# Kernel tuning notes

Hardware: AMD Instinct MI355X
Metric: run time of the kernel (lower is better)

The kernel has to match this reference:

```python
import jax, jax.numpy as jnp
import numpy as np

N_NODES = 100000
IN_CH = 128
OUT_CH = 128
N_EDGES = 1700000


def setup_inputs() -> dict:
    key = jax.random.key(0)
    k_x, k_e, k_w = jax.random.split(key, 3)
    x = jax.random.normal(k_x, (N_NODES, IN_CH), dtype=jnp.float32)
    # edges: one self-loop per node (guarantees deg>=1 for every node),
    # remainder random
    loops = jnp.stack([jnp.arange(N_NODES, dtype=jnp.int64)] * 2)  # [2, N]
    rand = jax.random.randint(k_e, (2, N_EDGES - N_NODES), 0, N_NODES, dtype=jnp.int64)
    edge_index = jnp.concatenate([loops, rand], axis=1)  # [2, E]
    # glorot-uniform weight, zero bias (reset_parameters)
    limit = float(np.sqrt(6.0 / (IN_CH + OUT_CH)))
    weight = jax.random.uniform(k_w, (IN_CH, OUT_CH), dtype=jnp.float32,
                                minval=-limit, maxval=limit)
    bias = jnp.zeros((OUT_CH,), dtype=jnp.float32)
    return {"x": x, "edge_index": edge_index, "weight": weight, "bias": bias}


def reference(x, edge_index, weight, bias):
    row, col = edge_index[0], edge_index[1]
    # deg = bincount(row) over all N nodes
    deg = jax.ops.segment_sum(jnp.ones_like(row, dtype=jnp.float32), row,
                              num_segments=x.shape[0])
    deg_inv_sqrt = deg ** -0.5  # symmetric normalization
    norm = deg_inv_sqrt[row] * deg_inv_sqrt[col]  # [E]
    support = x @ weight  # [N, out]
    msgs = norm[:, None] * support[col]  # [E, out] gather + scale
    out = jax.ops.segment_sum(msgs, row, num_segments=x.shape[0])  # scatter-add
    return out + bias
```

## Files before the change

### kernel.cpp

```cpp
#include <hip/hip_runtime.h>
#include <hip/hip_bf16.h>


#define SCAN_B 256
#define NBLK_P 256
#define BSHIFT 9
#define NPB    512

typedef __attribute__((ext_vector_type(8))) short bf16x8;
typedef __attribute__((ext_vector_type(4))) float f32x4;

__device__ __forceinline__ uint32_t f2bf_rne(float f) {
    uint32_t u = __float_as_uint(f);
    return (u + 0x7fffu + ((u >> 16) & 1u)) >> 16;
}
__device__ __forceinline__ float bf_lo(uint32_t u) { return __uint_as_float(u << 16); }
__device__ __forceinline__ float bf_hi(uint32_t u) { return __uint_as_float(u & 0xffff0000u); }

__device__ __forceinline__ bf16x8 pack8(float4 lo, float4 hi) {
    union { bf16x8 v; ushort u[8]; } r;
    r.u[0] = (ushort)f2bf_rne(lo.x);
    r.u[1] = (ushort)f2bf_rne(lo.y);
    r.u[2] = (ushort)f2bf_rne(lo.z);
    r.u[3] = (ushort)f2bf_rne(lo.w);
    r.u[4] = (ushort)f2bf_rne(hi.x);
    r.u[5] = (ushort)f2bf_rne(hi.y);
    r.u[6] = (ushort)f2bf_rne(hi.z);
    r.u[7] = (ushort)f2bf_rne(hi.w);
    return r.v;
}

__global__ void wconv_kernel(const float* __restrict__ W, ushort* __restrict__ Wt) {
    int t = blockIdx.x * blockDim.x + threadIdx.x;
    int n = t >> 7, k = t & 127;
    Wt[n * 128 + k] = (ushort)f2bf_rne(W[k * 128 + n]);
}

__global__ __launch_bounds__(256) void mfma_gemm(const float* __restrict__ X,
                                                 const ushort* __restrict__ Wt,
                                                 uint32_t* __restrict__ S, int N) {
    const int wave = threadIdx.x >> 6;
    const int lane = threadIdx.x & 63;
    const int c16  = lane & 15;
    const int kg   = lane >> 4;
    const int row0 = blockIdx.x * 128 + wave * 32;

    int rA0 = row0 + c16;
    int rA1 = row0 + 16 + c16;
    if (rA0 >= N) rA0 = N - 1;
    if (rA1 >= N) rA1 = N - 1;

    f32x4 acc[2][8];
#pragma unroll
    for (int m = 0; m < 2; ++m)
#pragma unroll
        for (int cb = 0; cb < 8; ++cb) acc[m][cb] = (f32x4){0.f, 0.f, 0.f, 0.f};

    const float*  xa0 = X + (size_t)rA0 * 128 + kg * 8;
    const float*  xa1 = X + (size_t)rA1 * 128 + kg * 8;
    const ushort* wb  = Wt + kg * 8 + c16 * 128;

#pragma unroll
    for (int kk = 0; kk < 4; ++kk) {
        float4 a0lo = *(const float4*)(xa0 + kk * 32);
        float4 a0hi = *(const float4*)(xa0 + kk * 32 + 4);
        float4 a1lo = *(const float4*)(xa1 + kk * 32);
        float4 a1hi = *(const float4*)(xa1 + kk * 32 + 4);
        bf16x8 A0 = pack8(a0lo, a0hi);
        bf16x8 A1 = pack8(a1lo, a1hi);
#pragma unroll
        for (int cb = 0; cb < 8; ++cb) {
            bf16x8 B = *(const bf16x8*)(wb + (size_t)cb * 16 * 128 + kk * 32);
            acc[0][cb] = __builtin_amdgcn_mfma_f32_16x16x32_bf16(A0, B, acc[0][cb], 0, 0, 0);
            acc[1][cb] = __builtin_amdgcn_mfma_f32_16x16x32_bf16(A1, B, acc[1][cb], 0, 0, 0);
        }
    }
#pragma unroll
    for (int m = 0; m < 2; ++m) {
#pragma unroll
        for (int i = 0; i < 4; ++i) {
            int gr = row0 + m * 16 + kg * 4 + i;
            if (gr < N) {
#pragma unroll
                for (int cb = 0; cb < 4; ++cb) {
                    uint32_t p = f2bf_rne(acc[m][cb][i]) |
                                 (f2bf_rne(acc[m][cb + 4][i]) << 16);
                    S[(size_t)gr * 64 + cb * 16 + c16] = p;
                }
            }
        }
    }
}

__global__ __launch_bounds__(256) void p1_count(const int* __restrict__ row,
                                                int* __restrict__ cnt,
                                                int E, int chunk, int nbuck) {
    __shared__ int h[256];
    const int blk = blockIdx.x, t = threadIdx.x;
    for (int i = t; i < nbuck; i += 256) h[i] = 0;
    __syncthreads();
    int lo = blk * chunk, hi = min(E, lo + chunk);
    for (int e = lo + t; e < hi; e += 256) atomicAdd(&h[row[e] >> BSHIFT], 1);
    __syncthreads();
    for (int b = t; b < nbuck; b += 256) cnt[b * NBLK_P + blk] = h[b];
}

__global__ void scan_block_kernel(const int* __restrict__ in, int* __restrict__ outp,
                                  int* __restrict__ bsum, int M) {
    __shared__ int s[SCAN_B];
    int t = threadIdx.x;
    int g = blockIdx.x * SCAN_B + t;
    int v = (g < M) ? in[g] : 0;
    s[t] = v;
    __syncthreads();
#pragma unroll
    for (int off = 1; off < SCAN_B; off <<= 1) {
        int u = (t >= off) ? s[t - off] : 0;
        __syncthreads();
        s[t] += u;
        __syncthreads();
    }
    if (g < M) outp[g] = s[t] - v;
    if (t == SCAN_B - 1) bsum[blockIdx.x] = s[t];
}

__global__ void scan_bsum_kernel(int* __restrict__ bsum, int NB) {
    __shared__ int s[1024];
    int t = threadIdx.x;
    int v = (t < NB) ? bsum[t] : 0;
    s[t] = v;
    __syncthreads();
#pragma unroll
    for (int off = 1; off < 1024; off <<= 1) {
        int u = (t >= off) ? s[t - off] : 0;
        __syncthreads();
        s[t] += u;
        __syncthreads();
    }
    if (t < NB) bsum[t] = s[t] - v;
}

__global__ void scan_add_kernel(int* __restrict__ outp, const int* __restrict__ bsum, int M) {
    int g = blockIdx.x * blockDim.x + threadIdx.x;
    if (g < M) outp[g] += bsum[g >> 8];
}

__global__ __launch_bounds__(256) void p2_scatter(const int* __restrict__ row,
                                                  const int* __restrict__ col,
                                                  const int* __restrict__ off,
                                                  uint32_t* __restrict__ part,
                                                  int E, int chunk, int nbuck) {
    __shared__ int cur[256];
    const int blk = blockIdx.x, t = threadIdx.x;
    for (int b = t; b < nbuck; b += 256) cur[b] = off[b * NBLK_P + blk];
    __syncthreads();
    int lo = blk * chunk, hi = min(E, lo + chunk);
    for (int e = lo + t; e < hi; e += 256) {
        int r = row[e], c = col[e];
        int pos = atomicAdd(&cur[r >> BSHIFT], 1);
        part[pos] = ((uint32_t)(r & (NPB - 1)) << 17) | (uint32_t)c;
    }
}

__global__ __launch_bounds__(256) void p3_build(const uint32_t* __restrict__ part,
                                                const int* __restrict__ off,
                                                int* __restrict__ rowptr,
                                                float* __restrict__ dis,
                                                int* __restrict__ csr,
                                                int N, int E, int nbuck) {
    __shared__ int hist[NPB];
    __shared__ int lstart[NPB];
    __shared__ int s[256];
    const int b = blockIdx.x, t = threadIdx.x;
    const int base_node = b << BSHIFT;
    const int csr_base  = off[b * NBLK_P];
    const int end_b     = (b == nbuck - 1) ? E : off[(b + 1) * NBLK_P];

    for (int i = t; i < NPB; i += 256) hist[i] = 0;
    __syncthreads();
    for (int e = csr_base + t; e < end_b; e += 256)
        atomicAdd(&hist[part[e] >> 17], 1);
    __syncthreads();

    int a0 = hist[2 * t], a1 = hist[2 * t + 1];
    s[t] = a0 + a1;
    __syncthreads();
    int v = s[t];
#pragma unroll
    for (int o = 1; o < 256; o <<= 1) {
        int u = (t >= o) ? s[t - o] : 0;
        __syncthreads();
        s[t] += u;
        __syncthreads();
    }
    int ex = s[t] - v;
    lstart[2 * t]     = ex;
    lstart[2 * t + 1] = ex + a0;
    __syncthreads();

    for (int i = t; i < NPB; i += 256) {
        int node = base_node + i;
        if (node < N) {
            rowptr[node] = csr_base + lstart[i];
            dis[node]    = rsqrtf((float)hist[i]);
        }
    }
    __syncthreads();
    for (int i = t; i < NPB; i += 256) hist[i] = lstart[i];
    __syncthreads();
    for (int e = csr_base + t; e < end_b; e += 256) {
        uint32_t p = part[e];
        int pos = csr_base + atomicAdd(&hist[p >> 17], 1);
        csr[pos] = (int)(p & 0x1FFFFu);
    }
    if (b == 0 && t == 0) rowptr[N] = E;
}

__global__ __launch_bounds__(256) void gather_kernel(const int* __restrict__ csr,
                                                     const int* __restrict__ rowptr,
                                                     const float* __restrict__ dis,
                                                     const uint32_t* __restrict__ sup,
                                                     const float* __restrict__ bias,
                                                     float* __restrict__ out, int N) {
    int wid  = (blockIdx.x * blockDim.x + threadIdx.x) >> 6;
    int lane = threadIdx.x & 63;
    if (wid >= N) return;
    int begin = rowptr[wid];
    int end   = rowptr[wid + 1];
    float dr  = dis[wid];
    float2 acc;
    acc.x = bias[lane];
    acc.y = bias[64 + lane];

    int j = begin;
    for (; j + 3 < end; j += 4) {
        int c0 = csr[j], c1 = csr[j + 1], c2 = csr[j + 2], c3 = csr[j + 3];
        float n0 = dr * dis[c0], n1 = dr * dis[c1], n2 = dr * dis[c2], n3 = dr * dis[c3];
        uint32_t u0 = sup[(size_t)c0 * 64 + lane];
        uint32_t u1 = sup[(size_t)c1 * 64 + lane];
        uint32_t u2 = sup[(size_t)c2 * 64 + lane];
        uint32_t u3 = sup[(size_t)c3 * 64 + lane];
        acc.x += n0 * bf_lo(u0) + n1 * bf_lo(u1) + n2 * bf_lo(u2) + n3 * bf_lo(u3);
        acc.y += n0 * bf_hi(u0) + n1 * bf_hi(u1) + n2 * bf_hi(u2) + n3 * bf_hi(u3);
    }
    for (; j < end; ++j) {
        int c = csr[j];
        float nrm = dr * dis[c];
        uint32_t u = sup[(size_t)c * 64 + lane];
        acc.x += nrm * bf_lo(u);
        acc.y += nrm * bf_hi(u);
    }
    out[(size_t)wid * 128 + lane]      = acc.x;
    out[(size_t)wid * 128 + 64 + lane] = acc.y;
}

#define GB_M 64
#define GB_KC 32
__global__ __launch_bounds__(256) void gemm_kernel(const float* __restrict__ X,
                                                   const float* __restrict__ W,
                                                   uint32_t* __restrict__ S, int N) {
    __shared__ float sXT[GB_KC][72];
    __shared__ float sW[GB_KC][128];
    const int t  = threadIdx.x;
    const int tx = t & 15;
    const int ty = t >> 4;
    const int bm = blockIdx.x * GB_M;

    float acc[4][8];
#pragma unroll
    for (int i = 0; i < 4; ++i)
#pragma unroll
        for (int j = 0; j < 8; ++j) acc[i][j] = 0.f;

    const int sr = t >> 2;
    const int sc = (t & 3) << 2;

    for (int k0 = 0; k0 < 128; k0 += GB_KC) {
#pragma unroll
        for (int h = 0; h < 2; ++h) {
            int kk = sc + h * 16;
            int gr = bm + sr;
            float4 v = make_float4(0.f, 0.f, 0.f, 0.f);
            if (gr < N) v = *(const float4*)(X + (size_t)gr * 128 + k0 + kk);
            sXT[kk + 0][sr] = v.x;
            sXT[kk + 1][sr] = v.y;
            sXT[kk + 2][sr] = v.z;
            sXT[kk + 3][sr] = v.w;
        }
#pragma unroll
        for (int h = 0; h < 4; ++h) {
            int idx = t + h * 256;
            int wk  = idx >> 5;
            int wo  = (idx & 31) << 2;
            *(float4*)&sW[wk][wo] = *(const float4*)(W + (size_t)(k0 + wk) * 128 + wo);
        }
        __syncthreads();
#pragma unroll
        for (int k = 0; k < GB_KC; ++k) {
            float4 a  = *(const float4*)&sXT[k][ty * 4];
            float4 b0 = *(const float4*)&sW[k][tx * 4];
            float4 b1 = *(const float4*)&sW[k][64 + tx * 4];
            float av[4] = {a.x, a.y, a.z, a.w};
            float bv[8] = {b0.x, b0.y, b0.z, b0.w, b1.x, b1.y, b1.z, b1.w};
#pragma unroll
            for (int i = 0; i < 4; ++i)
#pragma unroll
                for (int j = 0; j < 8; ++j) acc[i][j] += av[i] * bv[j];
        }
        __syncthreads();
    }
#pragma unroll
    for (int i = 0; i < 4; ++i) {
        int gr = bm + ty * 4 + i;
        if (gr < N) {
            uint4 q;
            q.x = f2bf_rne(acc[i][0]) | (f2bf_rne(acc[i][4]) << 16);
            q.y = f2bf_rne(acc[i][1]) | (f2bf_rne(acc[i][5]) << 16);
            q.z = f2bf_rne(acc[i][2]) | (f2bf_rne(acc[i][6]) << 16);
            q.w = f2bf_rne(acc[i][3]) | (f2bf_rne(acc[i][7]) << 16);
            *(uint4*)(S + (size_t)gr * 64 + tx * 4) = q;
        }
    }
}

__global__ void deg_i_kernel(const int* __restrict__ row, int* __restrict__ degi, int E) {
    int g = blockIdx.x * blockDim.x + threadIdx.x;
    if (g < E) atomicAdd(&degi[row[g]], 1);
}
__global__ void rsqrt_i_kernel(const int* __restrict__ degi, float* __restrict__ dis, int N) {
    int g = blockIdx.x * blockDim.x + threadIdx.x;
    if (g < N) dis[g] = rsqrtf((float)degi[g]);
}
__global__ void fill_kernel(const int* __restrict__ row, const int* __restrict__ col,
                            int* __restrict__ start, int* __restrict__ csr, int E) {
    int e = blockIdx.x * blockDim.x + threadIdx.x;
    if (e < E) {
        int pos = atomicAdd(&start[row[e]], 1);
        csr[pos] = col[e];
    }
}
__global__ void rowptr_from_start_kernel(const int* __restrict__ startv,
                                         int* __restrict__ rowptr, int N, int E) {
    int g = blockIdx.x * blockDim.x + threadIdx.x;
    if (g < N) rowptr[g] = startv[g];
    if (g == 0) rowptr[N] = E;
}

extern "C" void kernel_launch(void* const* d_in, const int* in_sizes, int n_in,
                              void* d_out, int out_size, void* d_ws, size_t ws_size,
                              hipStream_t stream) {
    const float* x    = (const float*)d_in[0];
    const int*   ei   = (const int*)d_in[1];
    const float* W    = (const float*)d_in[2];
    const float* bias = (const float*)d_in[3];
    float*       out  = (float*)d_out;

    const int N = in_sizes[0] / 128;
    const int E = in_sizes[1] / 2;
    const int* row = ei;
    const int* col = ei + E;

    const int nbuck = (N + NPB - 1) >> BSHIFT;
    const int M     = nbuck * NBLK_P;
    const int chunk = (E + NBLK_P - 1) / NBLK_P;
    const int NBm   = (M + SCAN_B - 1) / SCAN_B;

    auto al = [](size_t v) { return (v + 511) & ~(size_t)511; };
    size_t o_cnt    = 0;
    size_t o_off    = al(o_cnt + (size_t)M * 4);
    size_t o_bsum   = al(o_off + (size_t)M * 4);
    size_t o_rowptr = al(o_bsum + 4096 * 4);
    size_t o_dis    = al(o_rowptr + ((size_t)N + 1) * 4);
    size_t o_csr    = al(o_dis + (size_t)N * 4);
    size_t o_part   = al(o_csr + (size_t)E * 4);
    size_t o_wt     = al(o_part + (size_t)E * 4);
    size_t o_sup    = al(o_wt + 128 * 128 * 2);
    size_t need     = o_sup + (size_t)N * 256;

    char* ws = (char*)d_ws;

    if (ws_size >= need && nbuck <= 256 && NBm <= 1024 && N <= (1 << 17)) {
        int*      cnt    = (int*)(ws + o_cnt);
        int*      off    = (int*)(ws + o_off);
        int*      bsum   = (int*)(ws + o_bsum);
        int*      rowptr = (int*)(ws + o_rowptr);
        float*    dis    = (float*)(ws + o_dis);
        int*      csr    = (int*)(ws + o_csr);
        uint32_t* part   = (uint32_t*)(ws + o_part);
        ushort*   wt     = (ushort*)(ws + o_wt);
        uint32_t* sup    = (uint32_t*)(ws + o_sup);

        wconv_kernel<<<64, 256, 0, stream>>>(W, wt);
        mfma_gemm<<<(N + 127) / 128, 256, 0, stream>>>(x, wt, sup, N);

        p1_count<<<NBLK_P, 256, 0, stream>>>(row, cnt, E, chunk, nbuck);
        scan_block_kernel<<<NBm, SCAN_B, 0, stream>>>(cnt, off, bsum, M);
        scan_bsum_kernel<<<1, 1024, 0, stream>>>(bsum, NBm);
        scan_add_kernel<<<NBm, SCAN_B, 0, stream>>>(off, bsum, M);
        p2_scatter<<<NBLK_P, 256, 0, stream>>>(row, col, off, part, E, chunk, nbuck);
        p3_build<<<nbuck, 256, 0, stream>>>(part, off, rowptr, dis, csr, N, E, nbuck);

        long long gthreads = (long long)N * 64;
        gather_kernel<<<(int)((gthreads + 255) / 256), 256, 0, stream>>>(
            csr, rowptr, dis, sup, bias, out, N);
    } else {
        size_t f_degi   = 0;
        size_t f_dis    = al(f_degi + (size_t)N * 4);
        size_t f_start  = al(f_dis + (size_t)N * 4);
        size_t f_rowptr = al(f_start + (size_t)N * 4);
        size_t f_bsum   = al(f_rowptr + ((size_t)N + 1) * 4);
        size_t f_csr    = al(f_bsum + 4096 * 4);
        size_t f_sup    = al(f_csr + (size_t)E * 4);

        int*      degi   = (int*)(ws + f_degi);
        float*    dis    = (float*)(ws + f_dis);
        int*      startv = (int*)(ws + f_start);
        int*      rowptr = (int*)(ws + f_rowptr);
        int*      bsum   = (int*)(ws + f_bsum);
        int*      csr    = (int*)(ws + f_csr);
        uint32_t* sup    = (uint32_t*)(ws + f_sup);
        const int NBn = (N + SCAN_B - 1) / SCAN_B;

        hipMemsetAsync(degi, 0, (size_t)N * 4, stream);
        gemm_kernel<<<(N + GB_M - 1) / GB_M, 256, 0, stream>>>(x, W, sup, N);
        deg_i_kernel<<<(E + 255) / 256, 256, 0, stream>>>(row, degi, E);
        scan_block_kernel<<<NBn, SCAN_B, 0, stream>>>(degi, startv, bsum, N);
        scan_bsum_kernel<<<1, 1024, 0, stream>>>(bsum, NBn);
        scan_add_kernel<<<NBn, SCAN_B, 0, stream>>>(startv, bsum, N);
        rowptr_from_start_kernel<<<NBn, SCAN_B, 0, stream>>>(startv, rowptr, N, E);
        rsqrt_i_kernel<<<NBn, SCAN_B, 0, stream>>>(degi, dis, N);
        fill_kernel<<<(E + 255) / 256, 256, 0, stream>>>(row, col, startv, csr, E);
        long long gthreads = (long long)N * 64;
        gather_kernel<<<(int)((gthreads + 255) / 256), 256, 0, stream>>>(
            csr, rowptr, dis, sup, bias, out, N);
    }
}
```

Measured before the change: 164.5 us.

## Split gather wavefront into four edge groups with 16-byte loads and shuffle reduction

The gather kernel now splits each 64-lane wavefront into four 16-lane groups. Each group handles a different edge and loads 16 bytes (8 bf16 values) per lane instead of 4 bytes, and the partial sums are combined with xor shuffles at the end. This is meant to cut the serial per-edge latency chain and issue fewer, wider memory requests per row, since average degree is about 17. In exchange it adds shuffle-reduction overhead, wastes lanes on clamped tail iterations, and leaves only a quarter of lanes writing the output.

```diff
diff --git a/kernel.cpp b/kernel.cpp
--- a/kernel.cpp
+++ b/kernel.cpp
@@ -219,39 +219,59 @@
 __global__ __launch_bounds__(256) void gather_kernel(const int* __restrict__ csr,
                                                      const int* __restrict__ rowptr,
                                                      const float* __restrict__ dis,
-                                                     const uint32_t* __restrict__ sup,
+                                                     const uint4* __restrict__ sup,
                                                      const float* __restrict__ bias,
                                                      float* __restrict__ out, int N) {
     int wid  = (blockIdx.x * blockDim.x + threadIdx.x) >> 6;
     int lane = threadIdx.x & 63;
     if (wid >= N) return;
+    const int grp = lane >> 4;
+    const int li  = lane & 15;
     int begin = rowptr[wid];
     int end   = rowptr[wid + 1];
     float dr  = dis[wid];
-    float2 acc;
-    acc.x = bias[lane];
-    acc.y = bias[64 + lane];
-
-    int j = begin;
-    for (; j + 3 < end; j += 4) {
-        int c0 = csr[j], c1 = csr[j + 1], c2 = csr[j + 2], c3 = csr[j + 3];
-        float n0 = dr * dis[c0], n1 = dr * dis[c1], n2 = dr * dis[c2], n3 = dr * dis[c3];
-        uint32_t u0 = sup[(size_t)c0 * 64 + lane];
-        uint32_t u1 = sup[(size_t)c1 * 64 + lane];
-        uint32_t u2 = sup[(size_t)c2 * 64 + lane];
-        uint32_t u3 = sup[(size_t)c3 * 64 + lane];
-        acc.x += n0 * bf_lo(u0) + n1 * bf_lo(u1) + n2 * bf_lo(u2) + n3 * bf_lo(u3);
-        acc.y += n0 * bf_hi(u0) + n1 * bf_hi(u1) + n2 * bf_hi(u2) + n3 * bf_hi(u3);
-    }
-    for (; j < end; ++j) {
-        int c = csr[j];
-        float nrm = dr * dis[c];
-        uint32_t u = sup[(size_t)c * 64 + lane];
-        acc.x += nrm * bf_lo(u);
-        acc.y += nrm * bf_hi(u);
-    }
-    out[(size_t)wid * 128 + lane]      = acc.x;
-    out[(size_t)wid * 128 + 64 + lane] = acc.y;
+
+    float4 aL = make_float4(0.f, 0.f, 0.f, 0.f);
+    float4 aH = make_float4(0.f, 0.f, 0.f, 0.f);
+
+    for (int j = begin; j < end; j += 8) {
+        int e0 = j + grp, e1 = j + 4 + grp;
+        int c0 = csr[min(e0, end - 1)];
+        int c1 = csr[min(e1, end - 1)];
+        float n0 = (e0 < end) ? dr * dis[c0] : 0.f;
+        float n1 = (e1 < end) ? dr * dis[c1] : 0.f;
+        uint4 u0 = sup[(size_t)c0 * 16 + li];
+        uint4 u1 = sup[(size_t)c1 * 16 + li];
+        aL.x += n0 * bf_lo(u0.x) + n1 * bf_lo(u1.x);
+        aL.y += n0 * bf_lo(u0.y) + n1 * bf_lo(u1.y);
+        aL.z += n0 * bf_lo(u0.z) + n1 * bf_lo(u1.z);
+        aL.w += n0 * bf_lo(u0.w) + n1 * bf_lo(u1.w);
+        aH.x += n0 * bf_hi(u0.x) + n1 * bf_hi(u1.x);
+        aH.y += n0 * bf_hi(u0.y) + n1 * bf_hi(u1.y);
+        aH.z += n0 * bf_hi(u0.z) + n1 * bf_hi(u1.z);
+        aH.w += n0 * bf_hi(u0.w) + n1 * bf_hi(u1.w);
+    }
+
+#pragma unroll
+    for (int off = 16; off < 64; off <<= 1) {
+        aL.x += __shfl_xor(aL.x, off);
+        aL.y += __shfl_xor(aL.y, off);
+        aL.z += __shfl_xor(aL.z, off);
+        aL.w += __shfl_xor(aL.w, off);
+        aH.x += __shfl_xor(aH.x, off);
+        aH.y += __shfl_xor(aH.y, off);
+        aH.z += __shfl_xor(aH.z, off);
+        aH.w += __shfl_xor(aH.w, off);
+    }
+
+    if (grp == 0) {
+        float4 bL = *(const float4*)(bias + li * 4);
+        float4 bH = *(const float4*)(bias + 64 + li * 4);
+        aL.x += bL.x; aL.y += bL.y; aL.z += bL.z; aL.w += bL.w;
+        aH.x += bH.x; aH.y += bH.y; aH.z += bH.z; aH.w += bH.w;
+        *(float4*)(out + (size_t)wid * 128 + li * 4)      = aL;
+        *(float4*)(out + (size_t)wid * 128 + 64 + li * 4) = aH;
+    }
 }
 
 #define GB_M 64
@@ -388,10 +408,10 @@
         int*      csr    = (int*)(ws + o_csr);
         uint32_t* part   = (uint32_t*)(ws + o_part);
         ushort*   wt     = (ushort*)(ws + o_wt);
-        uint32_t* sup    = (uint32_t*)(ws + o_sup);
+        uint4*    sup    = (uint4*)(ws + o_sup);
 
         wconv_kernel<<<64, 256, 0, stream>>>(W, wt);
-        mfma_gemm<<<(N + 127) / 128, 256, 0, stream>>>(x, wt, sup, N);
+        mfma_gemm<<<(N + 127) / 128, 256, 0, stream>>>(x, wt, (uint32_t*)sup, N);
 
         p1_count<<<NBLK_P, 256, 0, stream>>>(row, cnt, E, chunk, nbuck);
         scan_block_kernel<<<NBm, SCAN_B, 0, stream>>>(cnt, off, bsum, M);
@@ -418,11 +438,11 @@
         int*      rowptr = (int*)(ws + f_rowptr);
         int*      bsum   = (int*)(ws + f_bsum);
         int*      csr    = (int*)(ws + f_csr);
-        uint32_t* sup    = (uint32_t*)(ws + f_sup);
+        uint4*    sup    = (uint4*)(ws + f_sup);
         const int NBn = (N + SCAN_B - 1) / SCAN_B;
 
         hipMemsetAsync(degi, 0, (size_t)N * 4, stream);
-        gemm_kernel<<<(N + GB_M - 1) / GB_M, 256, 0, stream>>>(x, W, sup, N);
+        gemm_kernel<<<(N + GB_M - 1) / GB_M, 256, 0, stream>>>(x, W, (uint32_t*)sup, N);
         deg_i_kernel<<<(E + 255) / 256, 256, 0, stream>>>(row, degi, E);
         scan_block_kernel<<<NBn, SCAN_B, 0, stream>>>(degi, startv, bsum, N);
         scan_bsum_kernel<<<1, 1024, 0, stream>>>(bsum, NBn);
```

New measurement: 163.7 us. No clear change (-0.5%).
